# Performance work log

Hardware: AMD Instinct MI355X
Metric: run time of the kernel (lower is better)

The kernel has to match this reference:

```python
import jax, jax.numpy as jnp
import numpy as np

B, M, N, DC = 32, 4096, 8192, 10
NUM_ITERS = 8
TEMP = 0.01      # smooth_min temperature
ALPHA = 100.0    # smooth_sign sharpness
BIG = 100000000.0


def setup_inputs() -> dict:
    rng = np.random.default_rng(0)
    # regular Tanner graph: each check connects to DC distinct variables
    chk_nbrs = np.argpartition(rng.random((M, N)), DC, axis=1)[:, :DC].astype(np.int32)
    p = rng.uniform(1e-3, 0.05, N)
    prior_llr = np.log((1.0 - p) / p).astype(np.float32)
    gamma = (0.1 * rng.standard_normal(N)).astype(np.float32)
    syndromes = rng.integers(0, 2, size=(B, M)).astype(np.float32)
    return {
        "syndromes": jnp.asarray(syndromes),
        "prior_llr": jnp.asarray(prior_llr),
        "gamma": jnp.asarray(gamma),
        "chk_nbrs": jnp.asarray(chk_nbrs),
    }


def _bp(syndromes, prior_llr, gamma, chk_nbrs):
    b = syndromes.shape[0]
    m, dc = chk_nbrs.shape
    n = prior_llr.shape[0]
    eye = jnp.eye(dc, dtype=bool)                      # (dc, dc)
    syn_sgn = 1.0 - 2.0 * syndromes                    # (b, m)
    var_flat = chk_nbrs.reshape(-1)                    # (m*dc,)

    def check_update(v2c):
        # v2c: (b, m, dc) messages var->check along each check's edge list
        s = jnp.tanh(ALPHA * v2c)                      # smooth_sign
        a = jnp.abs(v2c)
        # leave-one-out product of signs: mask diagonal with 1.0
        prod_excl = jnp.prod(jnp.where(eye, 1.0, s[:, :, None, :]), axis=-1)   # (b, m, dc)
        # leave-one-out smooth_min: mask diagonal with BIG, softmin-weighted sum
        a_m = jnp.where(eye, BIG, a[:, :, None, :])                            # (b, m, dc, dc)
        min_excl = jnp.sum(a_m * jax.nn.softmax(-a_m / TEMP, axis=-1), axis=-1)
        return syn_sgn[:, :, None] * prod_excl * min_excl                      # (b, m, dc)

    def scatter_to_vars(c2v):
        # sum of incoming check->var messages per variable: (b, n)
        return jnp.zeros((b, n), c2v.dtype).at[:, var_flat].add(c2v.reshape(b, -1))

    # initial v2c messages = prior LLR of the source variable
    v2c = jnp.broadcast_to(prior_llr[chk_nbrs], (b, m, dc))

    # iteration 0: no memory term
    c2v = check_update(v2c)
    llrs = scatter_to_vars(c2v) + prior_llr[None, :]
    v2c = llrs[:, chk_nbrs] - c2v

    def step(carry, _):
        v2c, llrs = carry
        c2v = check_update(v2c)
        llrs = scatter_to_vars(c2v) + (1.0 - gamma)[None, :] * prior_llr[None, :] + gamma[None, :] * llrs
        v2c = llrs[:, chk_nbrs] - c2v
        return (v2c, llrs), None

    (_, llrs), _ = jax.lax.scan(jax.checkpoint(step), (v2c, llrs), None, length=NUM_ITERS - 1)
    return llrs


def reference(syndromes, prior_llr, gamma, chk_nbrs):
    return _bp(syndromes, prior_llr, gamma, chk_nbrs)
```

## Files before the change

### kernel.cpp

```cpp
#include <hip/hip_runtime.h>

#define B 32
#define M 4096
#define N 8192
#define DC 10
#define NUM_ITERS 8
#define INV_TEMP 100.0f
#define ALPHA 100.0f
#define NB (N * B)
#define MB (M * B)
#define NEDGE (M * DC)

__global__ __launch_bounds__(256) void prologue_kernel(
    const float* __restrict__ syn,
    const float* __restrict__ prior,
    const float* __restrict__ gamma,
    float* __restrict__ accumA,
    float* __restrict__ L,
    float* __restrict__ syn_t,
    float* __restrict__ pg)
{
    int idx = blockIdx.x * blockDim.x + threadIdx.x;
    if (idx < NB) {
        accumA[idx] = 0.0f;
        L[idx] = prior[idx >> 5];
    }
    if (idx < MB) {
        int b = idx & 31, m = idx >> 5;
        syn_t[idx] = 1.0f - 2.0f * syn[(size_t)b * M + m];
    }
    if (idx < N) pg[idx] = (1.0f - gamma[idx]) * prior[idx];
}

template <int KIND, bool WL>
__global__ __launch_bounds__(256) void check_kernel(
    const float*  __restrict__ syn_t,
    const float*  __restrict__ prior,
    const float*  __restrict__ pg,
    const float*  __restrict__ gamma,
    const int*    __restrict__ nbrs,
    const float*  __restrict__ R,
    float*        __restrict__ W,
    float*        __restrict__ Z,
    float*        __restrict__ L,
    float2*       __restrict__ S)
{
    int idx = blockIdx.x * blockDim.x + threadIdx.x;
    if (idx >= MB) return;
    const int b = idx & 31;
    const int m = idx >> 5;

    Z[idx] = 0.0f;
    Z[idx + MB] = 0.0f;

    const int* nr = nbrs + m * DC;
    float2* Sp = S + (size_t)(m * DC) * B + b;

    int nb[DC];
    #pragma unroll
    for (int i = 0; i < DC; ++i) nb[i] = nr[i];

    float v[DC], lv[DC];
    if (KIND == 0) {
        #pragma unroll
        for (int i = 0; i < DC; ++i) { v[i] = prior[nb[i]]; lv[i] = v[i]; }
    } else {
        #pragma unroll
        for (int i = 0; i < DC; ++i) {
            float2 st = Sp[(size_t)i * B];
            const int g = nb[i] * B + b;
            float l;
            if (KIND == 1) l = R[g] + prior[nb[i]];
            else           l = R[g] + pg[nb[i]] + gamma[nb[i]] * st.y;
            if (WL) L[g] = l;
            lv[i] = l;
            v[i] = l - st.x;
        }
    }

    float s[DC], a[DC];
    #pragma unroll
    for (int i = 0; i < DC; ++i) {
        a[i] = fabsf(v[i]);
        float tt = __expf(-2.0f * ALPHA * a[i]);
        float mag = (1.0f - tt) / (1.0f + tt);
        s[i] = copysignf(mag, v[i]);
    }

    float min1 = 3.4e38f, min2 = 3.4e38f;
    int am = 0;
    #pragma unroll
    for (int i = 0; i < DC; ++i) {
        if (a[i] < min1) { min2 = min1; min1 = a[i]; am = i; }
        else if (a[i] < min2) { min2 = a[i]; }
    }

    float pre[DC + 1], suf[DC + 1];
    pre[0] = 1.0f;
    #pragma unroll
    for (int i = 0; i < DC; ++i) pre[i + 1] = pre[i] * s[i];
    suf[DC] = 1.0f;
    #pragma unroll
    for (int i = DC - 1; i >= 0; --i) suf[i] = suf[i + 1] * s[i];

    float w[DC];
    float se = 0.0f, sae = 0.0f;
    #pragma unroll
    for (int i = 0; i < DC; ++i) {
        w[i] = __expf((min1 - a[i]) * INV_TEMP);
        se  += w[i];
        sae += a[i] * w[i];
    }

    float se2 = 0.0f, sae2 = 0.0f;
    #pragma unroll
    for (int j = 0; j < DC; ++j) {
        float e2 = __expf((min2 - a[j]) * INV_TEMP);
        e2 = (j != am) ? e2 : 0.0f;
        se2  += e2;
        sae2 += a[j] * e2;
    }
    float me_am = sae2 / se2;

    float ssgn = syn_t[idx];

    #pragma unroll
    for (int i = 0; i < DC; ++i) {
        float me = (i == am) ? me_am : (sae - a[i] * w[i]) / (se - w[i]);
        float out = ssgn * (pre[i] * suf[i + 1]) * me;
        Sp[(size_t)i * B] = make_float2(out, lv[i]);
        atomicAdd(&W[nb[i] * B + b], out);
    }
}

__global__ __launch_bounds__(256) void final_kernel(
    const float* __restrict__ R,
    const float* __restrict__ pg,
    const float* __restrict__ gamma,
    const float* __restrict__ L,
    float*       __restrict__ out)
{
    int idx = blockIdx.x * blockDim.x + threadIdx.x;
    if (idx >= NB) return;
    int n = idx & (N - 1);
    int b = idx >> 13;
    int goff = n * B + b;
    out[idx] = R[goff] + pg[n] + gamma[n] * L[goff];
}

extern "C" void kernel_launch(void* const* d_in, const int* in_sizes, int n_in,
                              void* d_out, int out_size, void* d_ws, size_t ws_size,
                              hipStream_t stream) {
    const float* syn   = (const float*)d_in[0];
    const float* prior = (const float*)d_in[1];
    const float* gamma = (const float*)d_in[2];
    const int*   nbrs  = (const int*)d_in[3];
    float* out = (float*)d_out;

    float* ws = (float*)d_ws;
    float* A[3] = { ws, ws + NB, ws + 2 * (size_t)NB };
    float* L    = ws + 3 * (size_t)NB;
    float* syn_t= L + NB;
    float* pg   = syn_t + MB;
    float2* S   = (float2*)(pg + N);

    dim3 blk(256);
    dim3 pgrid((NB + 255) / 256);
    dim3 cgrid((MB + 255) / 256);

    prologue_kernel<<<pgrid, blk, 0, stream>>>(syn, prior, gamma, A[0], L, syn_t, pg);

    for (int t = 0; t < NUM_ITERS; ++t) {
        float* Rb = A[(t + 2) % 3];
        float* Wb = A[t % 3];
        float* Zb = A[(t + 1) % 3];
        if (t == 0) {
            check_kernel<0, false><<<cgrid, blk, 0, stream>>>(syn_t, prior, pg, gamma, nbrs,
                                                              Rb, Wb, Zb, L, S);
        } else if (t == 1) {
            check_kernel<1, false><<<cgrid, blk, 0, stream>>>(syn_t, prior, pg, gamma, nbrs,
                                                              Rb, Wb, Zb, L, S);
        } else if (t < NUM_ITERS - 1) {
            check_kernel<2, false><<<cgrid, blk, 0, stream>>>(syn_t, prior, pg, gamma, nbrs,
                                                              Rb, Wb, Zb, L, S);
        } else {
            check_kernel<2, true><<<cgrid, blk, 0, stream>>>(syn_t, prior, pg, gamma, nbrs,
                                                             Rb, Wb, Zb, L, S);
        }
    }
    final_kernel<<<pgrid, blk, 0, stream>>>(A[1], pg, gamma, L, out);
}
```

Baseline: 84.08 us.

## Split each check node's edges across two half-wavefronts with shuffle reductions

The check kernel now assigns each check node to 64 lanes instead of 32. Each 32-lane half handles 5 of the 10 edges for all 32 batch entries, and the two halves combine the sign product, the min1/min2/argmin and the softmin sums through __shfl_xor with offset 32. This doubles the thread count and halves the per-thread edge arrays, aiming for more wavefronts in flight and fewer registers, with launch_bounds set to ask for 4 blocks. The cost is extra cross-lane shuffles and a little duplicated reduction work. The zeroing of the next accumulation buffer is redistributed to one element per thread to match the larger grid.

```diff
diff --git a/kernel.cpp b/kernel.cpp
--- a/kernel.cpp
+++ b/kernel.cpp
@@ -33,7 +33,7 @@
 }
 
 template <int KIND, bool WL>
-__global__ __launch_bounds__(256) void check_kernel(
+__global__ __launch_bounds__(256, 4) void check_kernel(
     const float*  __restrict__ syn_t,
     const float*  __restrict__ prior,
     const float*  __restrict__ pg,
@@ -45,28 +45,28 @@
     float*        __restrict__ L,
     float2*       __restrict__ S)
 {
-    int idx = blockIdx.x * blockDim.x + threadIdx.x;
-    if (idx >= MB) return;
-    const int b = idx & 31;
-    const int m = idx >> 5;
-
-    Z[idx] = 0.0f;
-    Z[idx + MB] = 0.0f;
-
-    const int* nr = nbrs + m * DC;
-    float2* Sp = S + (size_t)(m * DC) * B + b;
-
-    int nb[DC];
-    #pragma unroll
-    for (int i = 0; i < DC; ++i) nb[i] = nr[i];
-
-    float v[DC], lv[DC];
+    const int tid  = threadIdx.x;
+    const int lane = tid & 63;
+    const int b    = lane & 31;
+    const int h    = lane >> 5;
+    const int m    = (blockIdx.x << 2) | (tid >> 6);
+
+    Z[blockIdx.x * 256 + tid] = 0.0f;
+
+    const int* nr = nbrs + m * DC + 5 * h;
+    float2* Sp = S + ((size_t)(m * DC + 5 * h)) * B + b;
+
+    int nb[5];
+    #pragma unroll
+    for (int i = 0; i < 5; ++i) nb[i] = nr[i];
+
+    float v[5], lv[5];
     if (KIND == 0) {
         #pragma unroll
-        for (int i = 0; i < DC; ++i) { v[i] = prior[nb[i]]; lv[i] = v[i]; }
+        for (int i = 0; i < 5; ++i) { v[i] = prior[nb[i]]; lv[i] = v[i]; }
     } else {
         #pragma unroll
-        for (int i = 0; i < DC; ++i) {
+        for (int i = 0; i < 5; ++i) {
             float2 st = Sp[(size_t)i * B];
             const int g = nb[i] * B + b;
             float l;
@@ -78,56 +78,73 @@
         }
     }
 
-    float s[DC], a[DC];
-    #pragma unroll
-    for (int i = 0; i < DC; ++i) {
+    float s[5], a[5];
+    #pragma unroll
+    for (int i = 0; i < 5; ++i) {
         a[i] = fabsf(v[i]);
         float tt = __expf(-2.0f * ALPHA * a[i]);
         float mag = (1.0f - tt) / (1.0f + tt);
         s[i] = copysignf(mag, v[i]);
     }
 
-    float min1 = 3.4e38f, min2 = 3.4e38f;
-    int am = 0;
-    #pragma unroll
-    for (int i = 0; i < DC; ++i) {
-        if (a[i] < min1) { min2 = min1; min1 = a[i]; am = i; }
-        else if (a[i] < min2) { min2 = a[i]; }
-    }
-
-    float pre[DC + 1], suf[DC + 1];
+    float pre[6], suf[6];
     pre[0] = 1.0f;
     #pragma unroll
-    for (int i = 0; i < DC; ++i) pre[i + 1] = pre[i] * s[i];
-    suf[DC] = 1.0f;
-    #pragma unroll
-    for (int i = DC - 1; i >= 0; --i) suf[i] = suf[i + 1] * s[i];
-
-    float w[DC];
-    float se = 0.0f, sae = 0.0f;
-    #pragma unroll
-    for (int i = 0; i < DC; ++i) {
-        w[i] = __expf((min1 - a[i]) * INV_TEMP);
+    for (int i = 0; i < 5; ++i) pre[i + 1] = pre[i] * s[i];
+    suf[5] = 1.0f;
+    #pragma unroll
+    for (int i = 4; i >= 0; --i) suf[i] = suf[i + 1] * s[i];
+    float prod_part = __shfl_xor(pre[5], 32, 64);
+
+    float m1o = 3.4e38f, m2o = 3.4e38f;
+    int amo = 0;
+    #pragma unroll
+    for (int i = 0; i < 5; ++i) {
+        if (a[i] < m1o) { m2o = m1o; m1o = a[i]; amo = i; }
+        else if (a[i] < m2o) { m2o = a[i]; }
+    }
+    int amo_g = amo + 5 * h;
+
+    float m1p   = __shfl_xor(m1o, 32, 64);
+    float m2p   = __shfl_xor(m2o, 32, 64);
+    int   amp_g = __shfl_xor(amo_g, 32, 64);
+
+    float m1_0 = h ? m1p : m1o,  m1_1 = h ? m1o : m1p;
+    int   am_0 = h ? amp_g : amo_g, am_1 = h ? amo_g : amp_g;
+    float min1g = fminf(m1_0, m1_1);
+    float min2g = fminf(fmaxf(m1_0, m1_1), fminf(m2o, m2p));
+    int   am_g  = (m1_0 <= m1_1) ? am_0 : am_1;
+
+    float w[5], se = 0.0f, sae = 0.0f;
+    #pragma unroll
+    for (int i = 0; i < 5; ++i) {
+        w[i] = __expf((min1g - a[i]) * INV_TEMP);
         se  += w[i];
         sae += a[i] * w[i];
     }
+    float se_tot  = se  + __shfl_xor(se, 32, 64);
+    float sae_tot = sae + __shfl_xor(sae, 32, 64);
 
     float se2 = 0.0f, sae2 = 0.0f;
     #pragma unroll
-    for (int j = 0; j < DC; ++j) {
-        float e2 = __expf((min2 - a[j]) * INV_TEMP);
-        e2 = (j != am) ? e2 : 0.0f;
+    for (int i = 0; i < 5; ++i) {
+        float e2 = __expf((min2g - a[i]) * INV_TEMP);
+        e2 = ((i + 5 * h) != am_g) ? e2 : 0.0f;
         se2  += e2;
-        sae2 += a[j] * e2;
-    }
-    float me_am = sae2 / se2;
-
-    float ssgn = syn_t[idx];
-
-    #pragma unroll
-    for (int i = 0; i < DC; ++i) {
-        float me = (i == am) ? me_am : (sae - a[i] * w[i]) / (se - w[i]);
-        float out = ssgn * (pre[i] * suf[i + 1]) * me;
+        sae2 += a[i] * e2;
+    }
+    float se2_tot  = se2  + __shfl_xor(se2, 32, 64);
+    float sae2_tot = sae2 + __shfl_xor(sae2, 32, 64);
+    float me_am = sae2_tot / se2_tot;
+
+    float ssgn = syn_t[(m << 5) | b];
+
+    #pragma unroll
+    for (int i = 0; i < 5; ++i) {
+        int gi = i + 5 * h;
+        float me = (gi == am_g) ? me_am
+                                : (sae_tot - a[i] * w[i]) / (se_tot - w[i]);
+        float out = ssgn * (pre[i] * suf[i + 1] * prod_part) * me;
         Sp[(size_t)i * B] = make_float2(out, lv[i]);
         atomicAdd(&W[nb[i] * B + b], out);
     }
@@ -166,7 +183,7 @@
 
     dim3 blk(256);
     dim3 pgrid((NB + 255) / 256);
-    dim3 cgrid((MB + 255) / 256);
+    dim3 cgrid(M / 4);
 
     prologue_kernel<<<pgrid, blk, 0, stream>>>(syn, prior, gamma, A[0], L, syn_t, pg);
 
```

Result: faster. 79.72 us (-5.2%).
